# Kernel tuning notes

Measured on AMD Instinct MI355X. Metric: run time of the kernel, lower is better.

## Reference

```python
import jax, jax.numpy as jnp
import numpy as np

PARALLEL = 4
EPS = 1e-5

# Binarization with sign (straight-through estimator in bwd; fwd is just sign)
@jax.custom_vjp
def binarize(x):
    return jnp.sign(x)

def _bin_fwd(x):
    return jnp.sign(x), x

def _bin_bwd(x, g):
    return (g * (jnp.abs(x) <= 1.0).astype(g.dtype),)

binarize.defvjp(_bin_fwd, _bin_bwd)


def bconv3x3(x, w, groups, stride=1):
    # XNOR-style conv: binarize activations and weights, grouped 3x3, pad 1
    return jax.lax.conv_general_dilated(
        binarize(x), binarize(w),
        window_strides=(stride, stride),
        padding=[(1, 1), (1, 1)],
        feature_group_count=groups,
        dimension_numbers=('NCHW', 'OIHW', 'NCHW'))


def batchnorm(x, scale, bias, mean, var):
    inv = scale * jax.lax.rsqrt(var + EPS)
    return x * inv[None, :, None, None] + (bias - mean * inv)[None, :, None, None]


def setup_inputs() -> dict:
    key = jax.random.key(0)
    ks = jax.random.split(key, 12)
    f32 = jnp.float32
    return {
        'x':         jax.random.normal(ks[0], (32, 256, 28, 28), dtype=f32),
        'w1':        jax.random.normal(ks[1], (1024, 256, 3, 3), dtype=f32),
        'bn1_scale': jax.random.uniform(ks[2], (1024,), dtype=f32),
        'bn1_bias':  jax.random.normal(ks[3], (1024,), dtype=f32),
        'bn1_mean':  jax.random.normal(ks[4], (1024,), dtype=f32),
        'bn1_var':   jax.random.uniform(ks[5], (1024,), dtype=f32),
        'w2':        jax.random.normal(ks[6], (1024, 256, 3, 3), dtype=f32),
        'bn2_scale': jax.random.uniform(ks[7], (1024,), dtype=f32),
        'bn2_bias':  jax.random.normal(ks[8], (1024,), dtype=f32),
        'bn2_mean':  jax.random.normal(ks[9], (1024,), dtype=f32),
        'bn2_var':   jax.random.uniform(ks[10], (1024,), dtype=f32),
        'lambdas':   jax.random.uniform(ks[11], (4,), dtype=f32),
    }


def reference(x, w1, bn1_scale, bn1_bias, bn1_mean, bn1_var,
              w2, bn2_scale, bn2_bias, bn2_mean, bn2_var, lambdas):
    identity = x  # downsample is None
    # squeeze: repeat channels parallel times -> [B, 1024, H, W]
    xr = jnp.tile(x, (1, PARALLEL, 1, 1))
    out = bconv3x3(xr, w1, groups=PARALLEL, stride=1)
    out = jax.nn.relu(batchnorm(out, bn1_scale, bn1_bias, bn1_mean, bn1_var))
    out = bconv3x3(out, w2, groups=PARALLEL, stride=1)
    out = batchnorm(out, bn2_scale, bn2_bias, bn2_mean, bn2_var)
    B, C, H, W = out.shape
    planes = C // PARALLEL
    # multiplication: per-group scalar lambda, broadcast over planes within each group
    out = out * jnp.repeat(lambdas, planes)[None, :, None, None]
    # squeeze: sum over parallel groups -> [B, planes, H, W]
    out = out.reshape(B, PARALLEL, planes, H, W).sum(axis=1)
    return jax.nn.relu(out + identity)
```

## Files before the change

### kernel.cpp

```cpp
#include <hip/hip_runtime.h>
#include <cstdint>

#define BN_EPS 1e-5f

typedef unsigned int uint;
typedef int v4i __attribute__((ext_vector_type(4)));
typedef int v16i __attribute__((ext_vector_type(16)));
typedef short v4h __attribute__((ext_vector_type(4)));


#define RSTR 7680
#define TILE4 30720

__global__ __launch_bounds__(256) void kPrep(
    const float* __restrict__ s1, const float* __restrict__ b1,
    const float* __restrict__ m1, const float* __restrict__ v1,
    const float* __restrict__ s2, const float* __restrict__ b2,
    const float* __restrict__ m2, const float* __restrict__ v2,
    const float* __restrict__ lam,
    float* __restrict__ thr1, float* __restrict__ bnA2,
    float* __restrict__ bbSum) {
  int t = blockIdx.x * 256 + threadIdx.x;
  if (t >= 1024) return;
  float inv1 = s1[t] / sqrtf(v1[t] + BN_EPS);
  float bb1 = b1[t] - m1[t] * inv1;
  thr1[t] = -bb1 / inv1;
  float inv2 = s2[t] / sqrtf(v2[t] + BN_EPS);
  bnA2[t] = inv2 * lam[t >> 8];
  if (t < 256) {
    float s = 0.f;
#pragma unroll
    for (int g = 0; g < 4; g++) {
      int i = g * 256 + t;
      float iv = s2[i] / sqrtf(v2[i] + BN_EPS);
      s += (b2[i] - m2[i] * iv) * lam[g];
    }
    bbSum[t] = s;
  }
}

__global__ __launch_bounds__(256) void kQ1(const float* __restrict__ x,
                                           char* __restrict__ A1i) {
  const int tid = threadIdx.x;
  const int lane = tid & 63, cb = tid >> 6;
  const int grp = blockIdx.x;
  const int b = grp / 49, p0 = (grp % 49) * 16;
  __shared__ char t[16][256];
  const float4* src =
      (const float4*)(x + ((size_t)(b * 256 + cb * 64 + lane) * 784 + p0));
  float4 f0 = src[0], f1 = src[1], f2 = src[2], f3 = src[3];
  const int c = cb * 64 + lane;
#define Q(V, J) t[J][c] = ((V) >= 0.f) ? (char)1 : (char)-1;
  Q(f0.x, 0)  Q(f0.y, 1)  Q(f0.z, 2)  Q(f0.w, 3)
  Q(f1.x, 4)  Q(f1.y, 5)  Q(f1.z, 6)  Q(f1.w, 7)
  Q(f2.x, 8)  Q(f2.y, 9)  Q(f2.z, 10) Q(f2.w, 11)
  Q(f3.x, 12) Q(f3.y, 13) Q(f3.z, 14) Q(f3.w, 15)
#undef Q
  __syncthreads();
  const int px = tid >> 4, ch = tid & 15;
  *(v4i*)(A1i + (size_t)(b * 784 + p0 + px) * 256 + ch * 16) =
      *(const v4i*)(&t[px][ch * 16]);
}

__global__ __launch_bounds__(256) void kWf(const float* __restrict__ w,
                                           char* __restrict__ Wf) {
  const int oc = blockIdx.x, ic = threadIdx.x;
  const float* s = w + (size_t)(oc * 256 + ic) * 9;
  const int ocb = oc >> 5;
  const int l = (oc & 31) + ((ic >> 4) & 1) * 32;
  const int kk = ic >> 5, j = ic & 15;
  char* base = Wf + (size_t)(ocb * 72 + kk) * 1024 + l * 16 + j;
#pragma unroll
  for (int tap = 0; tap < 9; tap++)
    base[(size_t)tap * 8 * 1024] = (s[tap] >= 0.f) ? (char)1 : (char)-1;
}

__global__ __launch_bounds__(256) void kConv1M(
    const char* __restrict__ A1i, const char* __restrict__ Wf1,
    const float* __restrict__ thr1, char* __restrict__ A2i) {
  const int tid = threadIdx.x;
  const int l = tid & 63, w = tid >> 6;
  const int xg = blockIdx.x;
  const int xcd = xg & 7, s = xg >> 3;
  const int b = xcd * 4 + (s & 3);
  const int rest = s >> 2;
  const int ocq = rest & 3, yt = rest >> 2;
  const int y0 = yt * 2;

  __shared__ char tile[TILE4];
  __shared__ float thrT[256];

  thrT[tid] = thr1[ocq * 256 + tid];
  {
    const v4i z = (v4i){0, 0, 0, 0};
    if (tid < 128) {
      int r = tid >> 5, j = tid & 31;
      int cl = (j & 1) ? 29 : 0, ch = j >> 1;
      *(v4i*)(tile + r * RSTR + cl * 256 + ((ch * 16) ^ ((cl & 15) << 4))) = z;
    }
#pragma unroll
    for (int r = 0; r < 4; r++) {
      int ry = y0 - 1 + r;
      if (ry < 0 || ry >= 28) {
        for (int i = tid; i < 448; i += 256) {
          int cl = (i >> 4) + 1, ch = i & 15;
          *(v4i*)(tile + r * RSTR + cl * 256 + ((ch * 16) ^ ((cl & 15) << 4))) = z;
        }
      }
    }
    const char* src = A1i + (size_t)b * 784 * 256;
    for (int i = tid; i < 1792; i += 256) {
      int r = i / 448, jj = i - r * 448;
      int px = jj >> 4, ch = jj & 15;
      int ry = y0 - 1 + r;
      if (ry >= 0 && ry < 28) {
        v4i v = *(const v4i*)(src + (size_t)(ry * 28 + px) * 256 + ch * 16);
        int cl = px + 1;
        *(v4i*)(tile + r * RSTR + cl * 256 + ((ch * 16) ^ ((cl & 15) << 4))) = v;
      }
    }
  }
  __syncthreads();

  const int col = l & 31, krow = l >> 5;
  int cbase[2], xm[2][3];
#pragma unroll
  for (int nb = 0; nb < 2; nb++) {
    int px = nb * 32 + col;
    int pxc = (px < 56) ? px : 55;
    int yy = pxc / 28, xx = pxc - yy * 28;
    cbase[nb] = yy * RSTR + xx * 256 + krow * 16;
#pragma unroll
    for (int e = 0; e < 3; e++) xm[nb][e] = ((xx + e) & 15) << 4;
  }

  v16i acc[2][2];
#pragma unroll
  for (int na = 0; na < 2; na++)
#pragma unroll
    for (int nb = 0; nb < 2; nb++) acc[na][nb] = (v16i)(0);
  const char* wb = Wf1 + (size_t)(ocq * 8 + w * 2) * 73728 + l * 16;

#pragma unroll
  for (int d = 0; d < 3; d++) {
#pragma unroll
    for (int e = 0; e < 3; e++) {
      const char* wp = wb + (size_t)(d * 3 + e) * 8192;
#pragma unroll
      for (int kk = 0; kk < 8; kk++) {
        v4i a0 = *(const v4i*)(wp + kk * 1024);
        v4i a1 = *(const v4i*)(wp + 73728 + kk * 1024);
#pragma unroll
        for (int nb = 0; nb < 2; nb++) {
          int baddr = cbase[nb] + d * RSTR + e * 256 + kk * 32;
          v4i bf = *(const v4i*)(tile + (baddr ^ xm[nb][e]));
          acc[0][nb] = __builtin_amdgcn_mfma_i32_32x32x32_i8(a0, bf, acc[0][nb], 0, 0, 0);
          acc[1][nb] = __builtin_amdgcn_mfma_i32_32x32x32_i8(a1, bf, acc[1][nb], 0, 0, 0);
        }
      }
    }
  }

  __syncthreads();
  char* bt = tile;
#pragma unroll
  for (int na = 0; na < 2; na++) {
#pragma unroll
    for (int nb = 0; nb < 2; nb++) {
      int px = nb * 32 + col;
      if (px < 56) {
#pragma unroll
        for (int qg = 0; qg < 4; qg++) {
          int ocb4 = w * 64 + na * 32 + qg * 8 + 4 * krow;
          float4 th = *(const float4*)&thrT[ocb4];
          uint word = 0;
          word |= ((float)acc[na][nb][qg * 4 + 0] > th.x) ? 0x01u : 0u;
          word |= ((float)acc[na][nb][qg * 4 + 1] > th.y) ? 0x100u : 0u;
          word |= ((float)acc[na][nb][qg * 4 + 2] > th.z) ? 0x10000u : 0u;
          word |= ((float)acc[na][nb][qg * 4 + 3] > th.w) ? 0x1000000u : 0u;
          *(uint*)(bt + px * 256 + (ocb4 ^ ((px & 15) << 4))) = word;
        }
      }
    }
  }
  __syncthreads();
  {
    char* dst = A2i + (size_t)(b * 784 + y0 * 28) * 1024 + ocq * 256;
    for (int i = tid; i < 896; i += 256) {
      int p2 = i >> 4, ch = i & 15;
      v4i v = *(const v4i*)(bt + p2 * 256 + ((ch * 16) ^ ((p2 & 15) << 4)));
      *(v4i*)(dst + (size_t)p2 * 1024 + ch * 16) = v;
    }
  }
}

__global__ __launch_bounds__(256) void kConv2P(
    const char* __restrict__ A2i, const char* __restrict__ Wf2,
    short* __restrict__ P16, int b0, int NBc) {
  const int tid = threadIdx.x;
  const int l = tid & 63, w = tid >> 6;
  const int xg = blockIdx.x;
  const int xcd = xg & 7, s = xg >> 3;
  const int g = xcd >> 1;
  const int bl = (s / 14) * 2 + (xcd & 1);
  const int yt = s % 14;
  const int b = b0 + bl;
  const int y0 = yt * 2;

  __shared__ char tile[TILE4];

  {
    const v4i z = (v4i){0, 0, 0, 0};
    if (tid < 128) {
      int r = tid >> 5, j = tid & 31;
      int cl = (j & 1) ? 29 : 0, ch = j >> 1;
      *(v4i*)(tile + r * RSTR + cl * 256 + ((ch * 16) ^ ((cl & 15) << 4))) = z;
    }
#pragma unroll
    for (int r = 0; r < 4; r++) {
      int ry = y0 - 1 + r;
      if (ry < 0 || ry >= 28) {
        for (int i = tid; i < 448; i += 256) {
          int cl = (i >> 4) + 1, ch = i & 15;
          *(v4i*)(tile + r * RSTR + cl * 256 + ((ch * 16) ^ ((cl & 15) << 4))) = z;
        }
      }
    }
    const char* src = A2i + (size_t)b * 784 * 1024 + g * 256;
    for (int i = tid; i < 1792; i += 256) {
      int r = i / 448, jj = i - r * 448;
      int px = jj >> 4, ch = jj & 15;
      int ry = y0 - 1 + r;
      if (ry >= 0 && ry < 28) {
        v4i v = *(const v4i*)(src + (size_t)(ry * 28 + px) * 1024 + ch * 16);
        int cl = px + 1;
        *(v4i*)(tile + r * RSTR + cl * 256 + ((ch * 16) ^ ((cl & 15) << 4))) = v;
      }
    }
  }
  __syncthreads();

  const int col = l & 31, krow = l >> 5;
  int cbase[2], xm[2][3];
#pragma unroll
  for (int nb = 0; nb < 2; nb++) {
    int px = nb * 32 + col;
    int pxc = (px < 56) ? px : 55;
    int yy = pxc / 28, xx = pxc - yy * 28;
    cbase[nb] = yy * RSTR + xx * 256 + krow * 16;
#pragma unroll
    for (int e = 0; e < 3; e++) xm[nb][e] = ((xx + e) & 15) << 4;
  }

  v16i acc[2][2];
#pragma unroll
  for (int na = 0; na < 2; na++)
#pragma unroll
    for (int nb = 0; nb < 2; nb++) acc[na][nb] = (v16i)(0);
  const char* wb = Wf2 + (size_t)(g * 8 + w * 2) * 73728 + l * 16;

#pragma unroll
  for (int d = 0; d < 3; d++) {
#pragma unroll
    for (int e = 0; e < 3; e++) {
      const char* wp = wb + (size_t)(d * 3 + e) * 8192;
#pragma unroll
      for (int kk = 0; kk < 8; kk++) {
        v4i a0 = *(const v4i*)(wp + kk * 1024);
        v4i a1 = *(const v4i*)(wp + 73728 + kk * 1024);
#pragma unroll
        for (int nb = 0; nb < 2; nb++) {
          int baddr = cbase[nb] + d * RSTR + e * 256 + kk * 32;
          v4i bf = *(const v4i*)(tile + (baddr ^ xm[nb][e]));
          acc[0][nb] = __builtin_amdgcn_mfma_i32_32x32x32_i8(a0, bf, acc[0][nb], 0, 0, 0);
          acc[1][nb] = __builtin_amdgcn_mfma_i32_32x32x32_i8(a1, bf, acc[1][nb], 0, 0, 0);
        }
      }
    }
  }

  short* base = P16 + ((size_t)((g * NBc + bl) * 784) + y0 * 28) * 256;
#pragma unroll
  for (int na = 0; na < 2; na++) {
#pragma unroll
    for (int nb = 0; nb < 2; nb++) {
      int px = nb * 32 + col;
      if (px < 56) {
        short* pp = base + px * 256 + w * 64 + na * 32 + 4 * krow;
#pragma unroll
        for (int qg = 0; qg < 4; qg++) {
          v4h v = {(short)acc[na][nb][qg * 4 + 0], (short)acc[na][nb][qg * 4 + 1],
                   (short)acc[na][nb][qg * 4 + 2], (short)acc[na][nb][qg * 4 + 3]};
          *(v4h*)(pp + 8 * qg) = v;
        }
      }
    }
  }
}

__global__ __launch_bounds__(256) void kRed(
    const short* __restrict__ P16, const float* __restrict__ bnA2,
    const float* __restrict__ bbSum, const float* __restrict__ xin,
    float* __restrict__ out, int b0, int NBc) {
  const int tid = threadIdx.x;
  const int y = blockIdx.x, bl = blockIdx.y, b = b0 + bl;

  __shared__ float vals[256 * 29];

  float cf[4];
#pragma unroll
  for (int g = 0; g < 4; g++) cf[g] = bnA2[g * 256 + tid];
  const float bbs = bbSum[tid];
  const short* Pp[4];
#pragma unroll
  for (int g = 0; g < 4; g++)
    Pp[g] = P16 + ((size_t)((g * NBc + bl) * 784) + y * 28) * 256 + tid;

  for (int x = 0; x < 28; x++) {
    float v = bbs;
#pragma unroll
    for (int g = 0; g < 4; g++)
      v += cf[g] * (float)(int)Pp[g][x * 256];
    vals[tid * 29 + x] = v;
  }
  __syncthreads();

#pragma unroll
  for (int k = 0; k < 7; k++) {
    int f = tid + 256 * k;
    int c = f / 7, xq = f - 7 * c;
    size_t base = ((size_t)(b * 256 + c) * 28 + y) * 28 + xq * 4;
    float4 xi = *(const float4*)(xin + base);
    float4 o;
    o.x = fmaxf(vals[c * 29 + xq * 4 + 0] + xi.x, 0.0f);
    o.y = fmaxf(vals[c * 29 + xq * 4 + 1] + xi.y, 0.0f);
    o.z = fmaxf(vals[c * 29 + xq * 4 + 2] + xi.z, 0.0f);
    o.w = fmaxf(vals[c * 29 + xq * 4 + 3] + xi.w, 0.0f);
    *(float4*)(out + base) = o;
  }
}

extern "C" void kernel_launch(void* const* d_in, const int* in_sizes, int n_in,
                              void* d_out, int out_size, void* d_ws, size_t ws_size,
                              hipStream_t stream) {
  const float* x   = (const float*)d_in[0];
  const float* w1  = (const float*)d_in[1];
  const float* s1  = (const float*)d_in[2];
  const float* b1  = (const float*)d_in[3];
  const float* m1  = (const float*)d_in[4];
  const float* v1  = (const float*)d_in[5];
  const float* w2  = (const float*)d_in[6];
  const float* s2  = (const float*)d_in[7];
  const float* b2  = (const float*)d_in[8];
  const float* m2  = (const float*)d_in[9];
  const float* v2  = (const float*)d_in[10];
  const float* lam = (const float*)d_in[11];
  float* out = (float*)d_out;

  char* ws = (char*)d_ws;
  char*  A1i   = ws + 0;
  char*  Wf1   = ws + 6422528;
  char*  Wf2   = ws + 8781824;
  char*  A2i   = ws + 11141120;
  float* thr1  = (float*)(ws + 36831232);
  float* bnA2  = (float*)(ws + 36835328);
  float* bbSum = (float*)(ws + 36839424);
  short* P16   = (short*)(ws + 36843520);

  const size_t needFull = 36843520ull + 4ull * 32 * 784 * 256 * 2;
  const int NBc = (ws_size >= needFull) ? 32 : 16;

  kPrep<<<4, 256, 0, stream>>>(s1, b1, m1, v1, s2, b2, m2, v2, lam,
                               thr1, bnA2, bbSum);
  kQ1<<<1568, 256, 0, stream>>>(x, A1i);
  kWf<<<1024, 256, 0, stream>>>(w1, Wf1);
  kWf<<<1024, 256, 0, stream>>>(w2, Wf2);
  kConv1M<<<1792, 256, 0, stream>>>(A1i, Wf1, thr1, A2i);
  for (int b0 = 0; b0 < 32; b0 += NBc) {
    kConv2P<<<8 * (NBc / 2) * 14, 256, 0, stream>>>(A2i, Wf2, P16, b0, NBc);
    kRed<<<dim3(28, NBc), 256, 0, stream>>>(P16, bnA2, bbSum, x, out, b0, NBc);
  }
}
```

Baseline: 193.0 us.

## Enlarge conv tiles to four output rows with 512-thread blocks

Both binary conv kernels now handle four output rows per block instead of two. They use 512 threads, split into two pixel halves that share the same four output-channel weight slices, and stage a 6-row halo tile in LDS. This cuts the redundant halo loads (6 rows loaded per 4 output rows instead of 4 per 2) and lets two waves reuse each weight-slice stream. In exchange each block uses more LDS and the grid has fewer blocks, which may lower occupancy.

```diff
diff --git a/kernel.cpp b/kernel.cpp
--- a/kernel.cpp
+++ b/kernel.cpp
@@ -10,7 +10,7 @@
 
 
 #define RSTR 7680
-#define TILE4 30720
+#define TILE6 46080
 
 __global__ __launch_bounds__(256) void kPrep(
     const float* __restrict__ s1, const float* __restrict__ b1,
@@ -75,41 +75,42 @@
     base[(size_t)tap * 8 * 1024] = (s[tap] >= 0.f) ? (char)1 : (char)-1;
 }
 
-__global__ __launch_bounds__(256) void kConv1M(
+__global__ __launch_bounds__(512) void kConv1M(
     const char* __restrict__ A1i, const char* __restrict__ Wf1,
     const float* __restrict__ thr1, char* __restrict__ A2i) {
   const int tid = threadIdx.x;
   const int l = tid & 63, w = tid >> 6;
+  const int wslice = w & 3, ph = w >> 2;
   const int xg = blockIdx.x;
   const int xcd = xg & 7, s = xg >> 3;
   const int b = xcd * 4 + (s & 3);
   const int rest = s >> 2;
   const int ocq = rest & 3, yt = rest >> 2;
-  const int y0 = yt * 2;
-
-  __shared__ char tile[TILE4];
+  const int y0 = yt * 4;
+
+  __shared__ char tile[TILE6];
   __shared__ float thrT[256];
 
-  thrT[tid] = thr1[ocq * 256 + tid];
+  if (tid < 256) thrT[tid] = thr1[ocq * 256 + tid];
   {
     const v4i z = (v4i){0, 0, 0, 0};
-    if (tid < 128) {
-      int r = tid >> 5, j = tid & 31;
+    if (tid < 192) {
+      int r = tid / 32, j = tid & 31;
       int cl = (j & 1) ? 29 : 0, ch = j >> 1;
       *(v4i*)(tile + r * RSTR + cl * 256 + ((ch * 16) ^ ((cl & 15) << 4))) = z;
     }
 #pragma unroll
-    for (int r = 0; r < 4; r++) {
+    for (int r = 0; r < 6; r++) {
       int ry = y0 - 1 + r;
       if (ry < 0 || ry >= 28) {
-        for (int i = tid; i < 448; i += 256) {
-          int cl = (i >> 4) + 1, ch = i & 15;
+        if (tid < 448) {
+          int cl = (tid >> 4) + 1, ch = tid & 15;
           *(v4i*)(tile + r * RSTR + cl * 256 + ((ch * 16) ^ ((cl & 15) << 4))) = z;
         }
       }
     }
     const char* src = A1i + (size_t)b * 784 * 256;
-    for (int i = tid; i < 1792; i += 256) {
+    for (int i = tid; i < 2688; i += 512) {
       int r = i / 448, jj = i - r * 448;
       int px = jj >> 4, ch = jj & 15;
       int ry = y0 - 1 + r;
@@ -126,8 +127,8 @@
   int cbase[2], xm[2][3];
 #pragma unroll
   for (int nb = 0; nb < 2; nb++) {
-    int px = nb * 32 + col;
-    int pxc = (px < 56) ? px : 55;
+    int px = ph * 64 + nb * 32 + col;
+    int pxc = (px < 112) ? px : 111;
     int yy = pxc / 28, xx = pxc - yy * 28;
     cbase[nb] = yy * RSTR + xx * 256 + krow * 16;
 #pragma unroll
@@ -139,7 +140,7 @@
   for (int na = 0; na < 2; na++)
 #pragma unroll
     for (int nb = 0; nb < 2; nb++) acc[na][nb] = (v16i)(0);
-  const char* wb = Wf1 + (size_t)(ocq * 8 + w * 2) * 73728 + l * 16;
+  const char* wb = Wf1 + (size_t)(ocq * 8 + wslice * 2) * 73728 + l * 16;
 
 #pragma unroll
   for (int d = 0; d < 3; d++) {
@@ -167,11 +168,11 @@
   for (int na = 0; na < 2; na++) {
 #pragma unroll
     for (int nb = 0; nb < 2; nb++) {
-      int px = nb * 32 + col;
-      if (px < 56) {
+      int px = ph * 64 + nb * 32 + col;
+      if (px < 112) {
 #pragma unroll
         for (int qg = 0; qg < 4; qg++) {
-          int ocb4 = w * 64 + na * 32 + qg * 8 + 4 * krow;
+          int ocb4 = wslice * 64 + na * 32 + qg * 8 + 4 * krow;
           float4 th = *(const float4*)&thrT[ocb4];
           uint word = 0;
           word |= ((float)acc[na][nb][qg * 4 + 0] > th.x) ? 0x01u : 0u;
@@ -186,7 +187,7 @@
   __syncthreads();
   {
     char* dst = A2i + (size_t)(b * 784 + y0 * 28) * 1024 + ocq * 256;
-    for (int i = tid; i < 896; i += 256) {
+    for (int i = tid; i < 1792; i += 512) {
       int p2 = i >> 4, ch = i & 15;
       v4i v = *(const v4i*)(bt + p2 * 256 + ((ch * 16) ^ ((p2 & 15) << 4)));
       *(v4i*)(dst + (size_t)p2 * 1024 + ch * 16) = v;
@@ -194,40 +195,41 @@
   }
 }
 
-__global__ __launch_bounds__(256) void kConv2P(
+__global__ __launch_bounds__(512) void kConv2P(
     const char* __restrict__ A2i, const char* __restrict__ Wf2,
     short* __restrict__ P16, int b0, int NBc) {
   const int tid = threadIdx.x;
   const int l = tid & 63, w = tid >> 6;
+  const int wslice = w & 3, ph = w >> 2;
   const int xg = blockIdx.x;
   const int xcd = xg & 7, s = xg >> 3;
   const int g = xcd >> 1;
-  const int bl = (s / 14) * 2 + (xcd & 1);
-  const int yt = s % 14;
+  const int bl = (s / 7) * 2 + (xcd & 1);
+  const int yt = s % 7;
   const int b = b0 + bl;
-  const int y0 = yt * 2;
-
-  __shared__ char tile[TILE4];
+  const int y0 = yt * 4;
+
+  __shared__ char tile[TILE6];
 
   {
     const v4i z = (v4i){0, 0, 0, 0};
-    if (tid < 128) {
-      int r = tid >> 5, j = tid & 31;
+    if (tid < 192) {
+      int r = tid / 32, j = tid & 31;
       int cl = (j & 1) ? 29 : 0, ch = j >> 1;
       *(v4i*)(tile + r * RSTR + cl * 256 + ((ch * 16) ^ ((cl & 15) << 4))) = z;
     }
 #pragma unroll
-    for (int r = 0; r < 4; r++) {
+    for (int r = 0; r < 6; r++) {
       int ry = y0 - 1 + r;
       if (ry < 0 || ry >= 28) {
-        for (int i = tid; i < 448; i += 256) {
-          int cl = (i >> 4) + 1, ch = i & 15;
+        if (tid < 448) {
+          int cl = (tid >> 4) + 1, ch = tid & 15;
           *(v4i*)(tile + r * RSTR + cl * 256 + ((ch * 16) ^ ((cl & 15) << 4))) = z;
         }
       }
     }
     const char* src = A2i + (size_t)b * 784 * 1024 + g * 256;
-    for (int i = tid; i < 1792; i += 256) {
+    for (int i = tid; i < 2688; i += 512) {
       int r = i / 448, jj = i - r * 448;
       int px = jj >> 4, ch = jj & 15;
       int ry = y0 - 1 + r;
@@ -244,8 +246,8 @@
   int cbase[2], xm[2][3];
 #pragma unroll
   for (int nb = 0; nb < 2; nb++) {
-    int px = nb * 32 + col;
-    int pxc = (px < 56) ? px : 55;
+    int px = ph * 64 + nb * 32 + col;
+    int pxc = (px < 112) ? px : 111;
     int yy = pxc / 28, xx = pxc - yy * 28;
     cbase[nb] = yy * RSTR + xx * 256 + krow * 16;
 #pragma unroll
@@ -257,7 +259,7 @@
   for (int na = 0; na < 2; na++)
 #pragma unroll
     for (int nb = 0; nb < 2; nb++) acc[na][nb] = (v16i)(0);
-  const char* wb = Wf2 + (size_t)(g * 8 + w * 2) * 73728 + l * 16;
+  const char* wb = Wf2 + (size_t)(g * 8 + wslice * 2) * 73728 + l * 16;
 
 #pragma unroll
   for (int d = 0; d < 3; d++) {
@@ -284,9 +286,9 @@
   for (int na = 0; na < 2; na++) {
 #pragma unroll
     for (int nb = 0; nb < 2; nb++) {
-      int px = nb * 32 + col;
-      if (px < 56) {
-        short* pp = base + px * 256 + w * 64 + na * 32 + 4 * krow;
+      int px = ph * 64 + nb * 32 + col;
+      if (px < 112) {
+        short* pp = base + px * 256 + wslice * 64 + na * 32 + 4 * krow;
 #pragma unroll
         for (int qg = 0; qg < 4; qg++) {
           v4h v = {(short)acc[na][nb][qg * 4 + 0], (short)acc[na][nb][qg * 4 + 1],
@@ -375,9 +377,9 @@
   kQ1<<<1568, 256, 0, stream>>>(x, A1i);
   kWf<<<1024, 256, 0, stream>>>(w1, Wf1);
   kWf<<<1024, 256, 0, stream>>>(w2, Wf2);
-  kConv1M<<<1792, 256, 0, stream>>>(A1i, Wf1, thr1, A2i);
+  kConv1M<<<896, 512, 0, stream>>>(A1i, Wf1, thr1, A2i);
   for (int b0 = 0; b0 < 32; b0 += NBc) {
-    kConv2P<<<8 * (NBc / 2) * 14, 256, 0, stream>>>(A2i, Wf2, P16, b0, NBc);
+    kConv2P<<<8 * (NBc / 2) * 7, 512, 0, stream>>>(A2i, Wf2, P16, b0, NBc);
     kRed<<<dim3(28, NBc), 256, 0, stream>>>(P16, bnA2, bbSum, x, out, b0, NBc);
   }
 }
```

Measured after the change: 185.8 us (median of 2 runs). 1.04x faster.

## Split conv pixel halves across extra waves with 512-thread blocks

Applied to the files above, without the earlier changes.

Both int8 MFMA conv kernels now run 8 waves per block instead of 4. Each wave handles one 32-pixel half of the tile instead of both, so accumulators drop from four 32x32 tiles to two per wave. This cuts register pressure and adds latency-hiding parallelism per CU. In exchange, weight fragments are loaded twice per block, once by each pixel-half wave, which doubles A-operand global/L2 traffic per block.

```diff
diff --git a/kernel.cpp b/kernel.cpp
--- a/kernel.cpp
+++ b/kernel.cpp
@@ -75,11 +75,12 @@
     base[(size_t)tap * 8 * 1024] = (s[tap] >= 0.f) ? (char)1 : (char)-1;
 }
 
-__global__ __launch_bounds__(256) void kConv1M(
+__global__ __launch_bounds__(512) void kConv1M(
     const char* __restrict__ A1i, const char* __restrict__ Wf1,
     const float* __restrict__ thr1, char* __restrict__ A2i) {
   const int tid = threadIdx.x;
   const int l = tid & 63, w = tid >> 6;
+  const int wslice = w & 3, ph = w >> 2;
   const int xg = blockIdx.x;
   const int xcd = xg & 7, s = xg >> 3;
   const int b = xcd * 4 + (s & 3);
@@ -90,7 +91,7 @@
   __shared__ char tile[TILE4];
   __shared__ float thrT[256];
 
-  thrT[tid] = thr1[ocq * 256 + tid];
+  if (tid < 256) thrT[tid] = thr1[ocq * 256 + tid];
   {
     const v4i z = (v4i){0, 0, 0, 0};
     if (tid < 128) {
@@ -102,14 +103,14 @@
     for (int r = 0; r < 4; r++) {
       int ry = y0 - 1 + r;
       if (ry < 0 || ry >= 28) {
-        for (int i = tid; i < 448; i += 256) {
-          int cl = (i >> 4) + 1, ch = i & 15;
+        if (tid < 448) {
+          int cl = (tid >> 4) + 1, ch = tid & 15;
           *(v4i*)(tile + r * RSTR + cl * 256 + ((ch * 16) ^ ((cl & 15) << 4))) = z;
         }
       }
     }
     const char* src = A1i + (size_t)b * 784 * 256;
-    for (int i = tid; i < 1792; i += 256) {
+    for (int i = tid; i < 1792; i += 512) {
       int r = i / 448, jj = i - r * 448;
       int px = jj >> 4, ch = jj & 15;
       int ry = y0 - 1 + r;
@@ -123,23 +124,18 @@
   __syncthreads();
 
   const int col = l & 31, krow = l >> 5;
-  int cbase[2], xm[2][3];
-#pragma unroll
-  for (int nb = 0; nb < 2; nb++) {
-    int px = nb * 32 + col;
-    int pxc = (px < 56) ? px : 55;
-    int yy = pxc / 28, xx = pxc - yy * 28;
-    cbase[nb] = yy * RSTR + xx * 256 + krow * 16;
-#pragma unroll
-    for (int e = 0; e < 3; e++) xm[nb][e] = ((xx + e) & 15) << 4;
-  }
-
-  v16i acc[2][2];
-#pragma unroll
-  for (int na = 0; na < 2; na++)
-#pragma unroll
-    for (int nb = 0; nb < 2; nb++) acc[na][nb] = (v16i)(0);
-  const char* wb = Wf1 + (size_t)(ocq * 8 + w * 2) * 73728 + l * 16;
+  const int px = ph * 32 + col;
+  const int pxc = (px < 56) ? px : 55;
+  const int yy = pxc / 28, xx = pxc - yy * 28;
+  const int cbase = yy * RSTR + xx * 256 + krow * 16;
+  int xm[3];
+#pragma unroll
+  for (int e = 0; e < 3; e++) xm[e] = ((xx + e) & 15) << 4;
+
+  v16i acc[2];
+  acc[0] = (v16i)(0);
+  acc[1] = (v16i)(0);
+  const char* wb = Wf1 + (size_t)(ocq * 8 + wslice * 2) * 73728 + l * 16;
 
 #pragma unroll
   for (int d = 0; d < 3; d++) {
@@ -150,43 +146,36 @@
       for (int kk = 0; kk < 8; kk++) {
         v4i a0 = *(const v4i*)(wp + kk * 1024);
         v4i a1 = *(const v4i*)(wp + 73728 + kk * 1024);
-#pragma unroll
-        for (int nb = 0; nb < 2; nb++) {
-          int baddr = cbase[nb] + d * RSTR + e * 256 + kk * 32;
-          v4i bf = *(const v4i*)(tile + (baddr ^ xm[nb][e]));
-          acc[0][nb] = __builtin_amdgcn_mfma_i32_32x32x32_i8(a0, bf, acc[0][nb], 0, 0, 0);
-          acc[1][nb] = __builtin_amdgcn_mfma_i32_32x32x32_i8(a1, bf, acc[1][nb], 0, 0, 0);
-        }
+        int baddr = cbase + d * RSTR + e * 256 + kk * 32;
+        v4i bf = *(const v4i*)(tile + (baddr ^ xm[e]));
+        acc[0] = __builtin_amdgcn_mfma_i32_32x32x32_i8(a0, bf, acc[0], 0, 0, 0);
+        acc[1] = __builtin_amdgcn_mfma_i32_32x32x32_i8(a1, bf, acc[1], 0, 0, 0);
       }
     }
   }
 
   __syncthreads();
   char* bt = tile;
-#pragma unroll
-  for (int na = 0; na < 2; na++) {
-#pragma unroll
-    for (int nb = 0; nb < 2; nb++) {
-      int px = nb * 32 + col;
-      if (px < 56) {
-#pragma unroll
-        for (int qg = 0; qg < 4; qg++) {
-          int ocb4 = w * 64 + na * 32 + qg * 8 + 4 * krow;
-          float4 th = *(const float4*)&thrT[ocb4];
-          uint word = 0;
-          word |= ((float)acc[na][nb][qg * 4 + 0] > th.x) ? 0x01u : 0u;
-          word |= ((float)acc[na][nb][qg * 4 + 1] > th.y) ? 0x100u : 0u;
-          word |= ((float)acc[na][nb][qg * 4 + 2] > th.z) ? 0x10000u : 0u;
-          word |= ((float)acc[na][nb][qg * 4 + 3] > th.w) ? 0x1000000u : 0u;
-          *(uint*)(bt + px * 256 + (ocb4 ^ ((px & 15) << 4))) = word;
-        }
+  if (px < 56) {
+#pragma unroll
+    for (int na = 0; na < 2; na++) {
+#pragma unroll
+      for (int qg = 0; qg < 4; qg++) {
+        int ocb4 = wslice * 64 + na * 32 + qg * 8 + 4 * krow;
+        float4 th = *(const float4*)&thrT[ocb4];
+        uint word = 0;
+        word |= ((float)acc[na][qg * 4 + 0] > th.x) ? 0x01u : 0u;
+        word |= ((float)acc[na][qg * 4 + 1] > th.y) ? 0x100u : 0u;
+        word |= ((float)acc[na][qg * 4 + 2] > th.z) ? 0x10000u : 0u;
+        word |= ((float)acc[na][qg * 4 + 3] > th.w) ? 0x1000000u : 0u;
+        *(uint*)(bt + px * 256 + (ocb4 ^ ((px & 15) << 4))) = word;
       }
     }
   }
   __syncthreads();
   {
     char* dst = A2i + (size_t)(b * 784 + y0 * 28) * 1024 + ocq * 256;
-    for (int i = tid; i < 896; i += 256) {
+    for (int i = tid; i < 896; i += 512) {
       int p2 = i >> 4, ch = i & 15;
       v4i v = *(const v4i*)(bt + p2 * 256 + ((ch * 16) ^ ((p2 & 15) << 4)));
       *(v4i*)(dst + (size_t)p2 * 1024 + ch * 16) = v;
@@ -194,11 +183,12 @@
   }
 }
 
-__global__ __launch_bounds__(256) void kConv2P(
+__global__ __launch_bounds__(512) void kConv2P(
     const char* __restrict__ A2i, const char* __restrict__ Wf2,
     short* __restrict__ P16, int b0, int NBc) {
   const int tid = threadIdx.x;
   const int l = tid & 63, w = tid >> 6;
+  const int wslice = w & 3, ph = w >> 2;
   const int xg = blockIdx.x;
   const int xcd = xg & 7, s = xg >> 3;
   const int g = xcd >> 1;
@@ -220,14 +210,14 @@
     for (int r = 0; r < 4; r++) {
       int ry = y0 - 1 + r;
       if (ry < 0 || ry >= 28) {
-        for (int i = tid; i < 448; i += 256) {
-          int cl = (i >> 4) + 1, ch = i & 15;
+        if (tid < 448) {
+          int cl = (tid >> 4) + 1, ch = tid & 15;
           *(v4i*)(tile + r * RSTR + cl * 256 + ((ch * 16) ^ ((cl & 15) << 4))) = z;
         }
       }
     }
     const char* src = A2i + (size_t)b * 784 * 1024 + g * 256;
-    for (int i = tid; i < 1792; i += 256) {
+    for (int i = tid; i < 1792; i += 512) {
       int r = i / 448, jj = i - r * 448;
       int px = jj >> 4, ch = jj & 15;
       int ry = y0 - 1 + r;
@@ -241,23 +231,18 @@
   __syncthreads();
 
   const int col = l & 31, krow = l >> 5;
-  int cbase[2], xm[2][3];
-#pragma unroll
-  for (int nb = 0; nb < 2; nb++) {
-    int px = nb * 32 + col;
-    int pxc = (px < 56) ? px : 55;
-    int yy = pxc / 28, xx = pxc - yy * 28;
-    cbase[nb] = yy * RSTR + xx * 256 + krow * 16;
-#pragma unroll
-    for (int e = 0; e < 3; e++) xm[nb][e] = ((xx + e) & 15) << 4;
-  }
-
-  v16i acc[2][2];
-#pragma unroll
-  for (int na = 0; na < 2; na++)
-#pragma unroll
-    for (int nb = 0; nb < 2; nb++) acc[na][nb] = (v16i)(0);
-  const char* wb = Wf2 + (size_t)(g * 8 + w * 2) * 73728 + l * 16;
+  const int px = ph * 32 + col;
+  const int pxc = (px < 56) ? px : 55;
+  const int yy = pxc / 28, xx = pxc - yy * 28;
+  const int cbase = yy * RSTR + xx * 256 + krow * 16;
+  int xm[3];
+#pragma unroll
+  for (int e = 0; e < 3; e++) xm[e] = ((xx + e) & 15) << 4;
+
+  v16i acc[2];
+  acc[0] = (v16i)(0);
+  acc[1] = (v16i)(0);
+  const char* wb = Wf2 + (size_t)(g * 8 + wslice * 2) * 73728 + l * 16;
 
 #pragma unroll
   for (int d = 0; d < 3; d++) {
@@ -268,31 +253,24 @@
       for (int kk = 0; kk < 8; kk++) {
         v4i a0 = *(const v4i*)(wp + kk * 1024);
         v4i a1 = *(const v4i*)(wp + 73728 + kk * 1024);
-#pragma unroll
-        for (int nb = 0; nb < 2; nb++) {
-          int baddr = cbase[nb] + d * RSTR + e * 256 + kk * 32;
-          v4i bf = *(const v4i*)(tile + (baddr ^ xm[nb][e]));
-          acc[0][nb] = __builtin_amdgcn_mfma_i32_32x32x32_i8(a0, bf, acc[0][nb], 0, 0, 0);
-          acc[1][nb] = __builtin_amdgcn_mfma_i32_32x32x32_i8(a1, bf, acc[1][nb], 0, 0, 0);
-        }
+        int baddr = cbase + d * RSTR + e * 256 + kk * 32;
+        v4i bf = *(const v4i*)(tile + (baddr ^ xm[e]));
+        acc[0] = __builtin_amdgcn_mfma_i32_32x32x32_i8(a0, bf, acc[0], 0, 0, 0);
+        acc[1] = __builtin_amdgcn_mfma_i32_32x32x32_i8(a1, bf, acc[1], 0, 0, 0);
       }
     }
   }
 
   short* base = P16 + ((size_t)((g * NBc + bl) * 784) + y0 * 28) * 256;
-#pragma unroll
-  for (int na = 0; na < 2; na++) {
-#pragma unroll
-    for (int nb = 0; nb < 2; nb++) {
-      int px = nb * 32 + col;
-      if (px < 56) {
-        short* pp = base + px * 256 + w * 64 + na * 32 + 4 * krow;
-#pragma unroll
-        for (int qg = 0; qg < 4; qg++) {
-          v4h v = {(short)acc[na][nb][qg * 4 + 0], (short)acc[na][nb][qg * 4 + 1],
-                   (short)acc[na][nb][qg * 4 + 2], (short)acc[na][nb][qg * 4 + 3]};
-          *(v4h*)(pp + 8 * qg) = v;
-        }
+  if (px < 56) {
+#pragma unroll
+    for (int na = 0; na < 2; na++) {
+      short* pp = base + px * 256 + wslice * 64 + na * 32 + 4 * krow;
+#pragma unroll
+      for (int qg = 0; qg < 4; qg++) {
+        v4h v = {(short)acc[na][qg * 4 + 0], (short)acc[na][qg * 4 + 1],
+                 (short)acc[na][qg * 4 + 2], (short)acc[na][qg * 4 + 3]};
+        *(v4h*)(pp + 8 * qg) = v;
       }
     }
   }
@@ -375,9 +353,9 @@
   kQ1<<<1568, 256, 0, stream>>>(x, A1i);
   kWf<<<1024, 256, 0, stream>>>(w1, Wf1);
   kWf<<<1024, 256, 0, stream>>>(w2, Wf2);
-  kConv1M<<<1792, 256, 0, stream>>>(A1i, Wf1, thr1, A2i);
+  kConv1M<<<1792, 512, 0, stream>>>(A1i, Wf1, thr1, A2i);
   for (int b0 = 0; b0 < 32; b0 += NBc) {
-    kConv2P<<<8 * (NBc / 2) * 14, 256, 0, stream>>>(A2i, Wf2, P16, b0, NBc);
+    kConv2P<<<8 * (NBc / 2) * 14, 512, 0, stream>>>(A2i, Wf2, P16, b0, NBc);
     kRed<<<dim3(28, NBc), 256, 0, stream>>>(P16, bnA2, bbSum, x, out, b0, NBc);
   }
 }
```

Result: slower. 215.5 us (+11.7%).
